# Optimization experiments

Measured on AMD Instinct MI355X. Metric: run time of the kernel, lower is better.

Reference implementation:

```python
import jax, jax.numpy as jnp
import numpy as np

N, E = 128, 2048
NODE_DIM, MSG_DIM, EDGE_DIM, ROUNDS, NUM_TYPES = 128, 128, 16, 2, 32


def setup_inputs() -> dict:
    key = jax.random.key(0)
    ks = jax.random.split(key, 10)
    s = 0.1  # weight scale to keep GRU numerics sane
    return {
        "node_types": jax.random.randint(ks[0], (N,), 0, NUM_TYPES),
        "src": jax.random.randint(ks[1], (E,), 0, N),
        "dst": jax.random.randint(ks[2], (E,), 0, N),
        "he": jax.random.normal(ks[3], (E, EDGE_DIM), jnp.float32),
        "enc_W": jax.random.normal(ks[4], (NODE_DIM, NUM_TYPES), jnp.float32) * s,
        "enc_b": jnp.zeros((NODE_DIM,), jnp.float32),
        "msg_W": jax.random.normal(ks[5], (ROUNDS, MSG_DIM, 2 * NODE_DIM + EDGE_DIM), jnp.float32) * s,
        "msg_b": jnp.zeros((ROUNDS, MSG_DIM), jnp.float32),
        "gru_Wih": jax.random.normal(ks[6], (ROUNDS, 3 * NODE_DIM, MSG_DIM), jnp.float32) * s,
        "gru_Whh": jax.random.normal(ks[7], (ROUNDS, 3 * NODE_DIM, NODE_DIM), jnp.float32) * s,
        "gru_bih": jnp.zeros((ROUNDS, 3 * NODE_DIM), jnp.float32),
        "gru_bhh": jnp.zeros((ROUNDS, 3 * NODE_DIM), jnp.float32),
        "cd_W": jax.random.normal(ks[8], (1, NODE_DIM), jnp.float32) * s,
        "cd_b": jnp.zeros((1,), jnp.float32),
    }


def _forward(node_types, src, dst, he, enc_W, enc_b, msg_W, msg_b,
             gru_Wih, gru_Whh, gru_bih, gru_bhh, cd_W, cd_b):
    n = node_types.shape[0]
    rounds = msg_W.shape[0]
    # initial_encoder on one-hot node types (g.ndata['out'].float())
    hv0 = jax.nn.one_hot(node_types, enc_W.shape[1], dtype=enc_W.dtype) @ enc_W.T + enc_b
    # fixed-key Gumbel noise emulating Categorical.sample() per destruction step
    gumbel = jax.random.gumbel(jax.random.key(42), (n - 1, n), dtype=hv0.dtype)

    def graph_prop(hv, alive):
        # DGL node removal emulated by alive mask; edges die with either endpoint
        emask = alive[src] & alive[dst]
        has_edges = emask.any()  # `if g.number_of_edges() > 0`
        emaskf = emask[:, None].astype(hv.dtype)
        upd = (has_edges & alive)[:, None]
        for t in range(rounds):
            m = jnp.concatenate([hv[src], hv[dst], he], axis=1)  # [E, 2d+e]
            m = (m @ msg_W[t].T + msg_b[t]) * emaskf             # [E, msg]
            a = jax.ops.segment_sum(m, dst, num_segments=n)      # [n, msg]; zero for no in-edges
            # torch.nn.GRUCell(a, hv), gate order r|z|n
            gi = a @ gru_Wih[t].T + gru_bih[t]
            gh = hv @ gru_Whh[t].T + gru_bhh[t]
            ir, iz, ih = jnp.split(gi, 3, axis=1)
            hr, hz, hn = jnp.split(gh, 3, axis=1)
            r = jax.nn.sigmoid(ir + hr)
            z = jax.nn.sigmoid(iz + hz)
            ncand = jnp.tanh(ih + r * hn)
            hv = jnp.where(upd, (1.0 - z) * ncand + z * hv, hv)
        return hv

    def step(carry, gn):
        hv, alive = carry
        hv = graph_prop(hv, alive)
        # softmax over dim=1 of [n,1] -> all ones (faithful to source); Categorical renormalizes
        probs = jax.nn.softmax(hv @ cd_W.T + cd_b, axis=1).reshape(-1)
        masked = probs * alive
        p = masked / masked.sum()
        vlog = jnp.where(alive, jnp.log(jnp.where(alive, p, 1.0)), -jnp.inf)
        victim = jnp.argmax(vlog + gn)  # Gumbel-max categorical sample
        logp = jnp.log(p[victim])
        alive = alive.at[victim].set(False)
        return (hv, alive), (victim, logp)

    alive0 = jnp.ones((n,), bool)
    (hv, alive), (victims, logps) = jax.lax.scan(step, (hv0, alive0), gumbel)
    survivor = jnp.argmax(alive)
    victim_order = jnp.concatenate([survivor[None], victims[::-1]])  # victim_order[::-1]
    return hv[survivor], victim_order, logps.sum()


def reference(node_types, src, dst, he, enc_W, enc_b, msg_W, msg_b,
              gru_Wih, gru_Whh, gru_bih, gru_bhh, cd_W, cd_b):
    return _forward(node_types, src, dst, he, enc_W, enc_b, msg_W, msg_b,
                    gru_Wih, gru_Whh, gru_bih, gru_bhh, cd_W, cd_b)
```

## Files before the change

kernel.cpp:

```cpp
#include <hip/hip_runtime.h>
#include <math.h>
#include <stdint.h>

#define STEPS 127
#define NBLK 64
#define NTHR 512
#define CAP 160

typedef unsigned int uint;

struct GDParams {
  const int* node_types; const int* esrc; const int* edst; const float* he;
  const float* enc_W; const float* enc_b; const float* msg_W; const float* msg_b;
  const float* Wih; const float* Whh; const float* bih; const float* bhh;
  unsigned* bar;
  unsigned* slots;
  float* buf0; float* buf1;
  float* g;
  unsigned short* Wp;
  float* W2T;
  float* bm2;
  float* HeSum;
  float* degs;
  unsigned char* alive;
  unsigned char* hasE;
  int* victims; int* row_ptr; int* in_count; int* cursor; int* col_src; int* col_eid;
  int* misc;
  float* out;
};

__device__ __forceinline__ void tfround(unsigned &x0, unsigned &x1, int r) {
  x0 += x1; x1 = (x1 << r) | (x1 >> (32 - r)); x1 ^= x0;
}
__device__ void threefry2x32(unsigned k0, unsigned k1, unsigned c0, unsigned c1,
                             unsigned &o0, unsigned &o1) {
  unsigned ks2 = k0 ^ k1 ^ 0x1BD11BDAu;
  unsigned x0 = c0 + k0, x1 = c1 + k1;
  tfround(x0,x1,13); tfround(x0,x1,15); tfround(x0,x1,26); tfround(x0,x1,6);
  x0 += k1; x1 += ks2 + 1u;
  tfround(x0,x1,17); tfround(x0,x1,29); tfround(x0,x1,16); tfround(x0,x1,24);
  x0 += ks2; x1 += k0 + 2u;
  tfround(x0,x1,13); tfround(x0,x1,15); tfround(x0,x1,26); tfround(x0,x1,6);
  x0 += k0; x1 += k1 + 3u;
  tfround(x0,x1,17); tfround(x0,x1,29); tfround(x0,x1,16); tfround(x0,x1,24);
  x0 += k1; x1 += ks2 + 4u;
  tfround(x0,x1,13); tfround(x0,x1,15); tfround(x0,x1,26); tfround(x0,x1,6);
  x0 += ks2; x1 += k0 + 5u;
  o0 = x0; o1 = x1;
}
__device__ __forceinline__ float gumbel_from_bits(unsigned b) {
  unsigned fb = (b >> 9) | 0x3F800000u;
  float f = __uint_as_float(fb) - 1.0f;
  const float tiny = 1.17549435e-38f;
  float u = fmaxf(tiny, f * (1.0f - tiny) + tiny);
  return -logf(-logf(u));
}

__device__ __forceinline__ unsigned short f2bf(float f) {
  unsigned u = __float_as_uint(f);
  unsigned r = (u + 0x7FFFu + ((u >> 16) & 1u)) >> 16;
  return (unsigned short)r;
}

#if __has_builtin(__builtin_amdgcn_fdot2_f32_bf16)
typedef __bf16 bf2 __attribute__((ext_vector_type(2)));
__device__ __forceinline__ float dot2bf(uint a, uint b, float c) {
  return __builtin_amdgcn_fdot2_f32_bf16(__builtin_bit_cast(bf2, a),
                                         __builtin_bit_cast(bf2, b), c, false);
}
#else
__device__ __forceinline__ float dot2bf(uint a, uint b, float c) {
  float a0 = __uint_as_float(a << 16), a1 = __uint_as_float(a & 0xFFFF0000u);
  float b0 = __uint_as_float(b << 16), b1 = __uint_as_float(b & 0xFFFF0000u);
  return fmaf(a0, b0, fmaf(a1, b1, c));
}
#endif

__device__ __forceinline__ float ld_dev(const float* a) {
  return __hip_atomic_load(const_cast<float*>(a), __ATOMIC_RELAXED, __HIP_MEMORY_SCOPE_AGENT);
}
__device__ __forceinline__ void st_dev(float* a, float v) {
  __hip_atomic_store(a, v, __ATOMIC_RELAXED, __HIP_MEMORY_SCOPE_AGENT);
}

__device__ __forceinline__ void gsync(unsigned* bar, unsigned &mygen) {
  __syncthreads();
  mygen++;
  if (threadIdx.x == 0) {
    unsigned prev = __hip_atomic_fetch_add(&bar[0], 1u, __ATOMIC_ACQ_REL, __HIP_MEMORY_SCOPE_AGENT);
    if (prev == (unsigned)(gridDim.x - 1u)) {
      __hip_atomic_store(&bar[0], 0u, __ATOMIC_RELAXED, __HIP_MEMORY_SCOPE_AGENT);
      __hip_atomic_store(&bar[1], mygen, __ATOMIC_RELEASE, __HIP_MEMORY_SCOPE_AGENT);
    } else {
      long guard = 0;
      while (__hip_atomic_load(&bar[1], __ATOMIC_ACQUIRE, __HIP_MEMORY_SCOPE_AGENT) != mygen) {
        if (++guard > (1L << 30)) break;
      }
    }
  }
  __syncthreads();
}

__device__ __forceinline__ void bpost(unsigned* slots, unsigned r) {
  __syncthreads();
  if (threadIdx.x == 0)
    __hip_atomic_store(&slots[blockIdx.x], r, __ATOMIC_RELAXED, __HIP_MEMORY_SCOPE_AGENT);
}
__device__ __forceinline__ void bwait(unsigned* slots, unsigned r) {
  if (threadIdx.x < 64) {
    long guard = 0;
    for (;;) {
      unsigned v = __hip_atomic_load(&slots[threadIdx.x], __ATOMIC_RELAXED, __HIP_MEMORY_SCOPE_AGENT);
      if (__all(v >= r)) break;
      if (++guard > (1L << 22)) break;
    }
  }
  __builtin_amdgcn_fence(__ATOMIC_ACQUIRE, "workgroup");
  __syncthreads();
}

__global__ __launch_bounds__(NTHR, 1) void gd_main(GDParams p) {
  __shared__ float pgq[4][2][384];
  __shared__ float pgr[2][2][384];
  __shared__ float pgh[2][2][384];
  __shared__ float pgHe[2][384];
  __shared__ alignas(16) unsigned short S_bf[2][128];
  __shared__ alignas(16) unsigned short hv_bf[2][128];
  __shared__ float hv_f[2][128];
  __shared__ int colL[2][CAP];
  __shared__ int cntL[2]; __shared__ int rpL[2];
  __shared__ float degL[2]; __shared__ int aliveL[2];
  __shared__ int victimL; __shared__ int hasEL;
  __shared__ int pfs[128];

  const int tid = threadIdx.x;
  const int gtid = blockIdx.x * NTHR + tid;
  const int GSZ = NBLK * NTHR;
  unsigned mygen = 0;

  if (blockIdx.x == 0) {
    for (int i = tid; i < 16256; i += NTHR) {
      unsigned o0, o1; threefry2x32(0u, 42u, 0u, (unsigned)i, o0, o1);
      p.g[i] = gumbel_from_bits(o0 ^ o1);
    }
    __syncthreads();
    if (tid < 64) {
      int lane = tid;
      bool a0 = true, a1 = true;
      float lsum = 0.f;
      for (int s = 0; s < STEPS; ++s) {
        p.alive[s * 128 + lane] = a0 ? 1 : 0;
        p.alive[s * 128 + 64 + lane] = a1 ? 1 : 0;
        float c = logf(1.0f / (float)(128 - s));
        float g0 = a0 ? (c + p.g[s * 128 + lane]) : -INFINITY;
        float g1 = a1 ? (c + p.g[s * 128 + 64 + lane]) : -INFINITY;
        float bv; int bi;
        if (g0 >= g1) { bv = g0; bi = lane; } else { bv = g1; bi = lane + 64; }
        for (int off = 32; off > 0; off >>= 1) {
          float ov = __shfl_down(bv, off);
          int   oi = __shfl_down(bi, off);
          if (ov > bv || (ov == bv && oi < bi)) { bv = ov; bi = oi; }
        }
        int victim = __shfl(bi, 0);
        if (victim == lane) a0 = false;
        if (victim == lane + 64) a1 = false;
        lsum += c;
        if (lane == 0) {
          p.victims[s] = victim;
          p.out[128 + 127 - s] = (float)victim;
        }
      }
      unsigned long long m0 = __ballot(a0), m1 = __ballot(a1);
      int surv = m0 ? (__ffsll(m0) - 1) : (64 + __ffsll(m1) - 1);
      if (lane == 0) { p.misc[0] = surv; p.out[128] = (float)surv; p.out[256] = lsum; }
    }
  } else {
    const int g63 = (blockIdx.x - 1) * NTHR + tid;
    const int GSZ63 = (NBLK - 1) * NTHR;
    for (int i = g63; i < 128; i += GSZ63) { p.in_count[i] = 0; p.cursor[i] = 0; }
    for (int i = g63; i < 16384; i += GSZ63) {
      int v = i >> 7, d = i & 127;
      p.buf0[i] = p.enc_W[d * 32 + p.node_types[v]] + p.enc_b[d];
    }
    for (int o = g63; o < 196608; o += GSZ63) {
      int mat = o / 98304; int r = o % 98304; int t = r / 49152; int rr = r % 49152;
      int k = rr / 384, j = rr % 384;
      const float* wih = p.Wih + (size_t)(t * 384 + j) * 128;
      const float* mw  = p.msg_W + (size_t)t * 128 * 272 + (mat * 128 + k);
      float acc = 0.f;
      for (int m = 0; m < 128; ++m) acc += wih[m] * mw[(size_t)m * 272];
      int mt = mat * 2 + t;
      p.Wp[(size_t)((mt * 16 + (k >> 3)) * 384 + j) * 8 + (k & 7)] = f2bf(acc);
    }
    for (int o = g63; o < 98304; o += GSZ63) {
      int t = o / 49152; int rr = o % 49152; int k = rr / 384, j = rr % 384;
      float acc = p.Whh[(size_t)(t * 384 + j) * 128 + k];
      int mt = 4 + t;
      p.Wp[(size_t)((mt * 16 + (k >> 3)) * 384 + j) * 8 + (k & 7)] = f2bf(acc);
    }
    for (int o = g63; o < 12288; o += GSZ63) {
      int t = o / 6144; int rr = o % 6144; int k = rr / 384, j = rr % 384;
      const float* wih = p.Wih + (size_t)(t * 384 + j) * 128;
      const float* mw  = p.msg_W + (size_t)t * 128 * 272 + (256 + k);
      float acc = 0.f;
      for (int m = 0; m < 128; ++m) acc += wih[m] * mw[(size_t)m * 272];
      p.W2T[(size_t)(t * 16 + k) * 384 + j] = acc;
    }
    for (int o = g63; o < 768; o += GSZ63) {
      int t = o / 384, j = o % 384;
      const float* wih = p.Wih + (size_t)(t * 384 + j) * 128;
      const float* mb = p.msg_b + t * 128;
      float acc = 0.f;
      for (int m = 0; m < 128; ++m) acc += wih[m] * mb[m];
      p.bm2[o] = acc;
    }
  }
  gsync(p.bar, mygen);

  if (blockIdx.x != 0) {
    for (int e = (blockIdx.x - 1) * NTHR + tid; e < 2048; e += (NBLK - 1) * NTHR)
      atomicAdd(&p.in_count[p.edst[e]], 1);
  }
  gsync(p.bar, mygen);

  if (blockIdx.x == 0) {
    if (tid < 128) pfs[tid] = p.in_count[tid];
    __syncthreads();
    for (int off = 1; off < 128; off <<= 1) {
      int add = 0;
      if (tid < 128 && tid >= off) add = pfs[tid - off];
      __syncthreads();
      if (tid < 128) pfs[tid] += add;
      __syncthreads();
    }
    if (tid == 0) p.row_ptr[0] = 0;
    if (tid < 128) p.row_ptr[tid + 1] = pfs[tid];
  }
  gsync(p.bar, mygen);

  for (int e = gtid; e < 2048; e += GSZ) {
    int dd = p.edst[e];
    int pos = atomicAdd(&p.cursor[dd], 1);
    int q = p.row_ptr[dd] + pos;
    p.col_src[q] = p.esrc[e];
    p.col_eid[q] = e;
  }
  gsync(p.bar, mygen);

  for (int i = gtid; i < 16256; i += GSZ) {
    int s = i >> 7, v = i & 127;
    int rp0 = p.row_ptr[v], rp1 = p.row_ptr[v + 1];
    const unsigned char* al = p.alive + s * 128;
    float deg = 0.f; float hacc[16];
    #pragma unroll
    for (int k = 0; k < 16; ++k) hacc[k] = 0.f;
    for (int q = rp0; q < rp1; ++q) {
      int u = p.col_src[q];
      if (al[u]) {
        deg += 1.f;
        const float* hr = p.he + (size_t)p.col_eid[q] * 16;
        #pragma unroll
        for (int k = 0; k < 16; ++k) hacc[k] += hr[k];
      }
    }
    p.degs[i] = deg;
    float* ho = p.HeSum + (size_t)i * 16;
    #pragma unroll
    for (int k = 0; k < 16; ++k) ho[k] = hacc[k];
  }
  gsync(p.bar, mygen);

  for (int s = gtid; s < STEPS; s += GSZ) {
    float acc = 0.f;
    for (int v = 0; v < 128; ++v)
      acc += p.alive[s * 128 + v] ? p.degs[s * 128 + v] : 0.f;
    p.hasE[s] = (acc > 0.f) ? 1 : 0;
  }
  for (int vv = 0; vv < 2; ++vv) {
    int v = blockIdx.x * 2 + vv;
    int rp0 = p.row_ptr[v], rp1 = p.row_ptr[v + 1];
    if (tid == 0) { cntL[vv] = rp1 - rp0; rpL[vv] = rp0; }
    int n = rp1 - rp0; if (n > CAP) n = CAP;
    for (int q = tid; q < n; q += NTHR) colL[vv][q] = p.col_src[rp0 + q];
  }
  gsync(p.bar, mygen);

  const float* cur = p.buf0; float* nxt = p.buf1;
  const int wave = tid >> 6, lane6 = tid & 63;
  const int nn = tid >> 7;
  const int dd_ = tid & 127;
  const int myv2 = blockIdx.x * 2;
  const uint4* Wp4 = (const uint4*)p.Wp;

  if (tid < 256) {
    float h0 = p.buf0[(size_t)(myv2 + nn) * 128 + dd_];
    hv_f[nn][dd_] = h0;
    hv_bf[nn][dd_] = f2bf(h0);
  }

  unsigned r = 0;
  for (int s = 0; s < STEPS; ++s) {
    for (int t = 0; t < 2; ++t) {
      r++;
      bpost(p.slots, r);

      if (wave >= 4) {
        const int m = 1 + ((wave - 4) >> 1);
        const int H = wave & 1;
        const uint4* WM = Wp4 + (size_t)(m * 2 + t) * 6144;
        float acc[6][2] = {};
        #pragma unroll
        for (int kc = 0; kc < 8; ++kc) {
          int kcg = H * 8 + kc;
          uint4 a0 = ((const uint4*)&hv_bf[0][0])[kcg];
          uint4 a1 = ((const uint4*)&hv_bf[1][0])[kcg];
          #pragma unroll
          for (int jj = 0; jj < 6; ++jj) {
            uint4 wv = WM[(size_t)kcg * 384 + lane6 + 64 * jj];
            acc[jj][0] = dot2bf(a0.x, wv.x, acc[jj][0]);
            acc[jj][0] = dot2bf(a0.y, wv.y, acc[jj][0]);
            acc[jj][0] = dot2bf(a0.z, wv.z, acc[jj][0]);
            acc[jj][0] = dot2bf(a0.w, wv.w, acc[jj][0]);
            acc[jj][1] = dot2bf(a1.x, wv.x, acc[jj][1]);
            acc[jj][1] = dot2bf(a1.y, wv.y, acc[jj][1]);
            acc[jj][1] = dot2bf(a1.z, wv.z, acc[jj][1]);
            acc[jj][1] = dot2bf(a1.w, wv.w, acc[jj][1]);
          }
        }
        float (*dst)[2][384] = (m == 1) ? pgr : pgh;
        #pragma unroll
        for (int jj = 0; jj < 6; ++jj) {
          dst[H][0][lane6 + 64 * jj] = acc[jj][0];
          dst[H][1][lane6 + 64 * jj] = acc[jj][1];
        }
        int base = tid - 256;
        #pragma unroll
        for (int ii = 0; ii < 3; ++ii) {
          int idx = base + 256 * ii;
          int n2 = (idx >= 384) ? 1 : 0;
          int j = idx - n2 * 384;
          int v = myv2 + n2;
          float deg = p.degs[s * 128 + v];
          float a = p.bih[t * 384 + j] + deg * p.bm2[t * 384 + j];
          const float* hs = p.HeSum + ((size_t)s * 128 + v) * 16;
          #pragma unroll
          for (int k2 = 0; k2 < 16; ++k2)
            a += hs[k2] * p.W2T[(size_t)(t * 16 + k2) * 384 + j];
          pgHe[n2][j] = a;
        }
      }

      bwait(p.slots, r);

      if (tid < 256) {
        if (tid == 0) { victimL = p.victims[s]; hasEL = p.hasE[s]; }
        if (dd_ == 0) {
          degL[nn] = p.degs[s * 128 + myv2 + nn];
          aliveL[nn] = p.alive[s * 128 + myv2 + nn];
        }
        float acc = 0.f;
        int cnt = cntL[nn];
        int cmin = cnt < CAP ? cnt : CAP;
        int q = 0;
        for (; q + 8 <= cmin; q += 8) {
          int u0 = colL[nn][q],   u1 = colL[nn][q+1], u2 = colL[nn][q+2], u3 = colL[nn][q+3];
          int u4 = colL[nn][q+4], u5 = colL[nn][q+5], u6 = colL[nn][q+6], u7 = colL[nn][q+7];
          float f0 = ld_dev(&cur[(size_t)u0*128 + dd_]);
          float f1 = ld_dev(&cur[(size_t)u1*128 + dd_]);
          float f2 = ld_dev(&cur[(size_t)u2*128 + dd_]);
          float f3 = ld_dev(&cur[(size_t)u3*128 + dd_]);
          float f4 = ld_dev(&cur[(size_t)u4*128 + dd_]);
          float f5 = ld_dev(&cur[(size_t)u5*128 + dd_]);
          float f6 = ld_dev(&cur[(size_t)u6*128 + dd_]);
          float f7 = ld_dev(&cur[(size_t)u7*128 + dd_]);
          acc += ((f0+f1)+(f2+f3)) + ((f4+f5)+(f6+f7));
        }
        for (; q < cnt; ++q) {
          int u = (q < CAP) ? colL[nn][q] : p.col_src[rpL[nn] + q];
          acc += ld_dev(&cur[(size_t)u*128 + dd_]);
        }
        S_bf[nn][dd_] = f2bf(acc);
      }
      __syncthreads();

      if (wave < 4) {
        const uint4* WQ = Wp4 + (size_t)(0 * 2 + t) * 6144;
        float acc[6][2] = {};
        #pragma unroll
        for (int kc = 0; kc < 4; ++kc) {
          int kcg = wave * 4 + kc;
          uint4 a0 = ((const uint4*)&S_bf[0][0])[kcg];
          uint4 a1 = ((const uint4*)&S_bf[1][0])[kcg];
          #pragma unroll
          for (int jj = 0; jj < 6; ++jj) {
            uint4 wv = WQ[(size_t)kcg * 384 + lane6 + 64 * jj];
            acc[jj][0] = dot2bf(a0.x, wv.x, acc[jj][0]);
            acc[jj][0] = dot2bf(a0.y, wv.y, acc[jj][0]);
            acc[jj][0] = dot2bf(a0.z, wv.z, acc[jj][0]);
            acc[jj][0] = dot2bf(a0.w, wv.w, acc[jj][0]);
            acc[jj][1] = dot2bf(a1.x, wv.x, acc[jj][1]);
            acc[jj][1] = dot2bf(a1.y, wv.y, acc[jj][1]);
            acc[jj][1] = dot2bf(a1.z, wv.z, acc[jj][1]);
            acc[jj][1] = dot2bf(a1.w, wv.w, acc[jj][1]);
          }
        }
        #pragma unroll
        for (int jj = 0; jj < 6; ++jj) {
          pgq[wave][0][lane6 + 64 * jj] = acc[jj][0];
          pgq[wave][1][lane6 + 64 * jj] = acc[jj][1];
        }
      }
      __syncthreads();

      if (tid < 256) {
        float deg = degL[nn];
        int j0 = dd_, j1 = 128 + dd_, j2 = 256 + dd_;
        float gir = pgq[0][nn][j0] + pgq[1][nn][j0] + pgq[2][nn][j0] + pgq[3][nn][j0]
                  + deg * (pgr[0][nn][j0] + pgr[1][nn][j0]) + pgHe[nn][j0];
        float giz = pgq[0][nn][j1] + pgq[1][nn][j1] + pgq[2][nn][j1] + pgq[3][nn][j1]
                  + deg * (pgr[0][nn][j1] + pgr[1][nn][j1]) + pgHe[nn][j1];
        float gin = pgq[0][nn][j2] + pgq[1][nn][j2] + pgq[2][nn][j2] + pgq[3][nn][j2]
                  + deg * (pgr[0][nn][j2] + pgr[1][nn][j2]) + pgHe[nn][j2];
        float ghr = pgh[0][nn][j0] + pgh[1][nn][j0] + p.bhh[t * 384 + j0];
        float ghz = pgh[0][nn][j1] + pgh[1][nn][j1] + p.bhh[t * 384 + j1];
        float ghn = pgh[0][nn][j2] + pgh[1][nn][j2] + p.bhh[t * 384 + j2];
        float rr_ = 1.f / (1.f + expf(-(gir + ghr)));
        float z = 1.f / (1.f + expf(-(giz + ghz)));
        float nc = tanhf(gin + rr_ * ghn);
        float old = hv_f[nn][dd_];
        bool upd = (hasEL != 0) && (aliveL[nn] != 0);
        float nv = upd ? (1.f - z) * nc + z * old : old;
        int myv = myv2 + nn;
        if (t == 1 && myv == victimL) nv = 0.f;
        st_dev(&nxt[(size_t)myv * 128 + dd_], nv);
        hv_f[nn][dd_] = nv;
        hv_bf[nn][dd_] = f2bf(nv);
      }
      const float* tmp = nxt; nxt = (float*)cur; cur = tmp;
    }
  }

  r++;
  bpost(p.slots, r);
  bwait(p.slots, r);
  if (blockIdx.x == 0 && tid < 128) {
    int surv = p.misc[0];
    p.out[tid] = ld_dev(&cur[(size_t)surv * 128 + tid]);
  }
}

extern "C" void kernel_launch(void* const* d_in, const int* in_sizes, int n_in,
                              void* d_out, int out_size, void* d_ws, size_t ws_size,
                              hipStream_t stream) {
  (void)in_sizes; (void)n_in; (void)out_size; (void)ws_size;
  GDParams p;
  p.node_types = (const int*)d_in[0];
  p.esrc = (const int*)d_in[1];
  p.edst = (const int*)d_in[2];
  p.he   = (const float*)d_in[3];
  p.enc_W = (const float*)d_in[4];
  p.enc_b = (const float*)d_in[5];
  p.msg_W = (const float*)d_in[6];
  p.msg_b = (const float*)d_in[7];
  p.Wih = (const float*)d_in[8];
  p.Whh = (const float*)d_in[9];
  p.bih = (const float*)d_in[10];
  p.bhh = (const float*)d_in[11];

  char* w = (char*)d_ws;
  auto take = [&](size_t n) { char* r = w; w += (n + 255) & ~(size_t)255; return r; };
  p.bar   = (unsigned*)take(256);
  p.slots = (unsigned*)take(256);
  p.buf0  = (float*)take(16384 * 4);
  p.buf1  = (float*)take(16384 * 4);
  p.g     = (float*)take(16256 * 4);
  p.Wp    = (unsigned short*)take((size_t)294912 * 2);
  p.W2T   = (float*)take(12288 * 4);
  p.bm2   = (float*)take(768 * 4);
  p.HeSum = (float*)take((size_t)16256 * 16 * 4);
  p.degs  = (float*)take(16256 * 4);
  p.alive = (unsigned char*)take(16384);
  p.hasE  = (unsigned char*)take(256);
  p.victims  = (int*)take(STEPS * 4);
  p.row_ptr  = (int*)take(129 * 4);
  p.in_count = (int*)take(128 * 4);
  p.cursor   = (int*)take(128 * 4);
  p.col_src  = (int*)take(2048 * 4);
  p.col_eid  = (int*)take(2048 * 4);
  p.misc     = (int*)take(256);
  p.out = (float*)d_out;

  (void)hipMemsetAsync(p.bar, 0, 512, stream);
  void* args[] = { (void*)&p };
  hipError_t err = hipLaunchCooperativeKernel(reinterpret_cast<void*>(gd_main),
                                              dim3(NBLK), dim3(NTHR), args, 0, stream);
  if (err != hipSuccess) {
    hipLaunchKernelGGL(gd_main, dim3(NBLK), dim3(NTHR), 0, stream, p);
  }
}
```

Before: 3.006 ms.

## Halve block count, pack hidden state as bf16, and early-exit finished blocks

New measurement: 4.410 ms. 46.7% more time.

```diff
diff --git a/kernel.cpp b/kernel.cpp
--- a/kernel.cpp
+++ b/kernel.cpp
@@ -3,7 +3,7 @@
 #include <stdint.h>
 
 #define STEPS 127
-#define NBLK 64
+#define NBLK 32
 #define NTHR 512
 #define CAP 160
 
@@ -15,7 +15,7 @@
   const float* Wih; const float* Whh; const float* bih; const float* bhh;
   unsigned* bar;
   unsigned* slots;
-  float* buf0; float* buf1;
+  uint* bufb0; uint* bufb1;
   float* g;
   unsigned short* Wp;
   float* W2T;
@@ -61,6 +61,8 @@
   unsigned r = (u + 0x7FFFu + ((u >> 16) & 1u)) >> 16;
   return (unsigned short)r;
 }
+__device__ __forceinline__ float bflo(uint w) { return __uint_as_float(w << 16); }
+__device__ __forceinline__ float bfhi(uint w) { return __uint_as_float(w & 0xFFFF0000u); }
 
 #if __has_builtin(__builtin_amdgcn_fdot2_f32_bf16)
 typedef __bf16 bf2 __attribute__((ext_vector_type(2)));
@@ -70,16 +72,14 @@
 }
 #else
 __device__ __forceinline__ float dot2bf(uint a, uint b, float c) {
-  float a0 = __uint_as_float(a << 16), a1 = __uint_as_float(a & 0xFFFF0000u);
-  float b0 = __uint_as_float(b << 16), b1 = __uint_as_float(b & 0xFFFF0000u);
-  return fmaf(a0, b0, fmaf(a1, b1, c));
+  return fmaf(bflo(a), bflo(b), fmaf(bfhi(a), bfhi(b), c));
 }
 #endif
 
-__device__ __forceinline__ float ld_dev(const float* a) {
-  return __hip_atomic_load(const_cast<float*>(a), __ATOMIC_RELAXED, __HIP_MEMORY_SCOPE_AGENT);
-}
-__device__ __forceinline__ void st_dev(float* a, float v) {
+__device__ __forceinline__ uint ld_devu(const uint* a) {
+  return __hip_atomic_load(const_cast<uint*>(a), __ATOMIC_RELAXED, __HIP_MEMORY_SCOPE_AGENT);
+}
+__device__ __forceinline__ void st_devu(uint* a, uint v) {
   __hip_atomic_store(a, v, __ATOMIC_RELAXED, __HIP_MEMORY_SCOPE_AGENT);
 }
 
@@ -108,11 +108,15 @@
 }
 __device__ __forceinline__ void bwait(unsigned* slots, unsigned r) {
   if (threadIdx.x < 64) {
+    int lane = threadIdx.x;
     long guard = 0;
     for (;;) {
-      unsigned v = __hip_atomic_load(&slots[threadIdx.x], __ATOMIC_RELAXED, __HIP_MEMORY_SCOPE_AGENT);
+      unsigned v = (lane < NBLK)
+        ? __hip_atomic_load(&slots[lane], __ATOMIC_RELAXED, __HIP_MEMORY_SCOPE_AGENT)
+        : 0xFFFFFFFFu;
       if (__all(v >= r)) break;
-      if (++guard > (1L << 22)) break;
+      __builtin_amdgcn_s_sleep(1);
+      if (++guard > (1L << 20)) break;
     }
   }
   __builtin_amdgcn_fence(__ATOMIC_ACQUIRE, "workgroup");
@@ -120,16 +124,16 @@
 }
 
 __global__ __launch_bounds__(NTHR, 1) void gd_main(GDParams p) {
-  __shared__ float pgq[4][2][384];
-  __shared__ float pgr[2][2][384];
-  __shared__ float pgh[2][2][384];
-  __shared__ float pgHe[2][384];
-  __shared__ alignas(16) unsigned short S_bf[2][128];
-  __shared__ alignas(16) unsigned short hv_bf[2][128];
-  __shared__ float hv_f[2][128];
-  __shared__ int colL[2][CAP];
-  __shared__ int cntL[2]; __shared__ int rpL[2];
-  __shared__ float degL[2]; __shared__ int aliveL[2];
+  __shared__ float pgq[4][4][384];
+  __shared__ float pgr[2][4][384];
+  __shared__ float pgh[2][4][384];
+  __shared__ float pgHe[4][384];
+  __shared__ alignas(16) uint S_u[4][64];
+  __shared__ alignas(16) uint hv_u[4][64];
+  __shared__ float hv_f[4][128];
+  __shared__ int colL[4][CAP];
+  __shared__ int cntL[4]; __shared__ int rpL[4];
+  __shared__ float degL[4]; __shared__ int aliveL[4];
   __shared__ int victimL; __shared__ int hasEL;
   __shared__ int pfs[128];
 
@@ -148,6 +152,7 @@
       int lane = tid;
       bool a0 = true, a1 = true;
       float lsum = 0.f;
+      p.misc[1 + lane] = 127; p.misc[1 + 64 + lane] = 127;
       for (int s = 0; s < STEPS; ++s) {
         p.alive[s * 128 + lane] = a0 ? 1 : 0;
         p.alive[s * 128 + 64 + lane] = a1 ? 1 : 0;
@@ -162,8 +167,8 @@
           if (ov > bv || (ov == bv && oi < bi)) { bv = ov; bi = oi; }
         }
         int victim = __shfl(bi, 0);
-        if (victim == lane) a0 = false;
-        if (victim == lane + 64) a1 = false;
+        if (victim == lane) { a0 = false; p.misc[1 + lane] = s; }
+        if (victim == lane + 64) { a1 = false; p.misc[1 + 64 + lane] = s; }
         lsum += c;
         if (lane == 0) {
           p.victims[s] = victim;
@@ -178,9 +183,12 @@
     const int g63 = (blockIdx.x - 1) * NTHR + tid;
     const int GSZ63 = (NBLK - 1) * NTHR;
     for (int i = g63; i < 128; i += GSZ63) { p.in_count[i] = 0; p.cursor[i] = 0; }
-    for (int i = g63; i < 16384; i += GSZ63) {
-      int v = i >> 7, d = i & 127;
-      p.buf0[i] = p.enc_W[d * 32 + p.node_types[v]] + p.enc_b[d];
+    for (int i = g63; i < 8192; i += GSZ63) {
+      int v = i >> 6, up = i & 63;
+      int ty = p.node_types[v];
+      float h0 = p.enc_W[(2 * up) * 32 + ty] + p.enc_b[2 * up];
+      float h1 = p.enc_W[(2 * up + 1) * 32 + ty] + p.enc_b[2 * up + 1];
+      p.bufb0[i] = (uint)f2bf(h0) | ((uint)f2bf(h1) << 16);
     }
     for (int o = g63; o < 196608; o += GSZ63) {
       int mat = o / 98304; int r = o % 98304; int t = r / 49152; int rr = r % 49152;
@@ -276,8 +284,8 @@
       acc += p.alive[s * 128 + v] ? p.degs[s * 128 + v] : 0.f;
     p.hasE[s] = (acc > 0.f) ? 1 : 0;
   }
-  for (int vv = 0; vv < 2; ++vv) {
-    int v = blockIdx.x * 2 + vv;
+  for (int vv = 0; vv < 4; ++vv) {
+    int v = blockIdx.x * 4 + vv;
     int rp0 = p.row_ptr[v], rp1 = p.row_ptr[v + 1];
     if (tid == 0) { cntL[vv] = rp1 - rp0; rpL[vv] = rp0; }
     int n = rp1 - rp0; if (n > CAP) n = CAP;
@@ -285,18 +293,28 @@
   }
   gsync(p.bar, mygen);
 
-  const float* cur = p.buf0; float* nxt = p.buf1;
+  const uint* curb = p.bufb0; uint* nxtb = p.bufb1;
   const int wave = tid >> 6, lane6 = tid & 63;
-  const int nn = tid >> 7;
-  const int dd_ = tid & 127;
-  const int myv2 = blockIdx.x * 2;
+  const int myv4 = blockIdx.x * 4;
   const uint4* Wp4 = (const uint4*)p.Wp;
 
-  if (tid < 256) {
-    float h0 = p.buf0[(size_t)(myv2 + nn) * 128 + dd_];
-    hv_f[nn][dd_] = h0;
-    hv_bf[nn][dd_] = f2bf(h0);
-  }
+  const int surv = p.misc[0];
+  int bexitS;
+  {
+    int m0 = p.misc[1 + myv4], m1 = p.misc[2 + myv4];
+    int m2 = p.misc[3 + myv4], m3 = p.misc[4 + myv4];
+    bexitS = max(max(m0, m1), max(m2, m3));
+  }
+
+  {
+    int n = tid >> 7, d = tid & 127;
+    int ty = p.node_types[myv4 + n];
+    float h0 = p.enc_W[d * 32 + ty] + p.enc_b[d];
+    hv_f[n][d] = h0;
+    float ph = __shfl_xor(h0, 1);
+    if ((tid & 1) == 0) hv_u[n][d >> 1] = (uint)f2bf(h0) | ((uint)f2bf(ph) << 16);
+  }
+  __syncthreads();
 
   unsigned r = 0;
   for (int s = 0; s < STEPS; ++s) {
@@ -304,16 +322,21 @@
       r++;
       bpost(p.slots, r);
 
-      if (wave >= 4) {
-        const int m = 1 + ((wave - 4) >> 1);
-        const int H = wave & 1;
-        const uint4* WM = Wp4 + (size_t)(m * 2 + t) * 6144;
+      if (tid == 0) { victimL = p.victims[s]; hasEL = p.hasE[s]; }
+      if (tid < 4) {
+        degL[tid] = p.degs[s * 128 + myv4 + tid];
+        aliveL[tid] = p.alive[s * 128 + myv4 + tid];
+      }
+      {
+        const int mm = wave & 1, H = (wave >> 1) & 1, P = wave >> 2;
+        const uint4* WM = Wp4 + (size_t)((mm ? 4 : 2) + t) * 6144;
+        const uint4* A0 = (const uint4*)&hv_u[P * 2][0];
+        const uint4* A1 = (const uint4*)&hv_u[P * 2 + 1][0];
         float acc[6][2] = {};
         #pragma unroll
         for (int kc = 0; kc < 8; ++kc) {
           int kcg = H * 8 + kc;
-          uint4 a0 = ((const uint4*)&hv_bf[0][0])[kcg];
-          uint4 a1 = ((const uint4*)&hv_bf[1][0])[kcg];
+          uint4 a0 = A0[kcg], a1 = A1[kcg];
           #pragma unroll
           for (int jj = 0; jj < 6; ++jj) {
             uint4 wv = WM[(size_t)kcg * 384 + lane6 + 64 * jj];
@@ -327,70 +350,72 @@
             acc[jj][1] = dot2bf(a1.w, wv.w, acc[jj][1]);
           }
         }
-        float (*dst)[2][384] = (m == 1) ? pgr : pgh;
+        float (*dst)[4][384] = mm ? pgh : pgr;
         #pragma unroll
         for (int jj = 0; jj < 6; ++jj) {
-          dst[H][0][lane6 + 64 * jj] = acc[jj][0];
-          dst[H][1][lane6 + 64 * jj] = acc[jj][1];
-        }
-        int base = tid - 256;
+          dst[H][P * 2][lane6 + 64 * jj] = acc[jj][0];
+          dst[H][P * 2 + 1][lane6 + 64 * jj] = acc[jj][1];
+        }
+      }
+      #pragma unroll
+      for (int ii = 0; ii < 3; ++ii) {
+        int idx = tid + 512 * ii;
+        int n2 = idx / 384, j = idx - n2 * 384;
+        int v = myv4 + n2;
+        float dg = p.degs[s * 128 + v];
+        float a = p.bih[t * 384 + j] + dg * p.bm2[t * 384 + j];
+        const float* hs = p.HeSum + ((size_t)s * 128 + v) * 16;
         #pragma unroll
-        for (int ii = 0; ii < 3; ++ii) {
-          int idx = base + 256 * ii;
-          int n2 = (idx >= 384) ? 1 : 0;
-          int j = idx - n2 * 384;
-          int v = myv2 + n2;
-          float deg = p.degs[s * 128 + v];
-          float a = p.bih[t * 384 + j] + deg * p.bm2[t * 384 + j];
-          const float* hs = p.HeSum + ((size_t)s * 128 + v) * 16;
-          #pragma unroll
-          for (int k2 = 0; k2 < 16; ++k2)
-            a += hs[k2] * p.W2T[(size_t)(t * 16 + k2) * 384 + j];
-          pgHe[n2][j] = a;
-        }
+        for (int k2 = 0; k2 < 16; ++k2)
+          a += hs[k2] * p.W2T[(size_t)(t * 16 + k2) * 384 + j];
+        pgHe[n2][j] = a;
       }
 
       bwait(p.slots, r);
 
-      if (tid < 256) {
-        if (tid == 0) { victimL = p.victims[s]; hasEL = p.hasE[s]; }
-        if (dd_ == 0) {
-          degL[nn] = p.degs[s * 128 + myv2 + nn];
-          aliveL[nn] = p.alive[s * 128 + myv2 + nn];
-        }
-        float acc = 0.f;
-        int cnt = cntL[nn];
+      {
+        int n = tid >> 7, u = (tid >> 1) & 63, e = tid & 1;
+        int cnt = cntL[n];
         int cmin = cnt < CAP ? cnt : CAP;
-        int q = 0;
-        for (; q + 8 <= cmin; q += 8) {
-          int u0 = colL[nn][q],   u1 = colL[nn][q+1], u2 = colL[nn][q+2], u3 = colL[nn][q+3];
-          int u4 = colL[nn][q+4], u5 = colL[nn][q+5], u6 = colL[nn][q+6], u7 = colL[nn][q+7];
-          float f0 = ld_dev(&cur[(size_t)u0*128 + dd_]);
-          float f1 = ld_dev(&cur[(size_t)u1*128 + dd_]);
-          float f2 = ld_dev(&cur[(size_t)u2*128 + dd_]);
-          float f3 = ld_dev(&cur[(size_t)u3*128 + dd_]);
-          float f4 = ld_dev(&cur[(size_t)u4*128 + dd_]);
-          float f5 = ld_dev(&cur[(size_t)u5*128 + dd_]);
-          float f6 = ld_dev(&cur[(size_t)u6*128 + dd_]);
-          float f7 = ld_dev(&cur[(size_t)u7*128 + dd_]);
-          acc += ((f0+f1)+(f2+f3)) + ((f4+f5)+(f6+f7));
-        }
-        for (; q < cnt; ++q) {
-          int u = (q < CAP) ? colL[nn][q] : p.col_src[rpL[nn] + q];
-          acc += ld_dev(&cur[(size_t)u*128 + dd_]);
-        }
-        S_bf[nn][dd_] = f2bf(acc);
+        float aL = 0.f, aH = 0.f;
+        int q = e;
+        for (; q + 14 < cmin; q += 16) {
+          int c0 = colL[n][q],      c1 = colL[n][q + 2],  c2 = colL[n][q + 4],  c3 = colL[n][q + 6];
+          int c4 = colL[n][q + 8],  c5 = colL[n][q + 10], c6 = colL[n][q + 12], c7 = colL[n][q + 14];
+          uint w0 = ld_devu(&curb[(size_t)c0 * 64 + u]);
+          uint w1 = ld_devu(&curb[(size_t)c1 * 64 + u]);
+          uint w2 = ld_devu(&curb[(size_t)c2 * 64 + u]);
+          uint w3 = ld_devu(&curb[(size_t)c3 * 64 + u]);
+          uint w4 = ld_devu(&curb[(size_t)c4 * 64 + u]);
+          uint w5 = ld_devu(&curb[(size_t)c5 * 64 + u]);
+          uint w6 = ld_devu(&curb[(size_t)c6 * 64 + u]);
+          uint w7 = ld_devu(&curb[(size_t)c7 * 64 + u]);
+          aL += ((bflo(w0) + bflo(w1)) + (bflo(w2) + bflo(w3)))
+              + ((bflo(w4) + bflo(w5)) + (bflo(w6) + bflo(w7)));
+          aH += ((bfhi(w0) + bfhi(w1)) + (bfhi(w2) + bfhi(w3)))
+              + ((bfhi(w4) + bfhi(w5)) + (bfhi(w6) + bfhi(w7)));
+        }
+        for (; q < cnt; q += 2) {
+          int c = (q < CAP) ? colL[n][q] : p.col_src[rpL[n] + q];
+          uint w = ld_devu(&curb[(size_t)c * 64 + u]);
+          aL += bflo(w); aH += bfhi(w);
+        }
+        aL += __shfl_xor(aL, 1);
+        aH += __shfl_xor(aH, 1);
+        if (e == 0) S_u[n][u] = (uint)f2bf(aL) | ((uint)f2bf(aH) << 16);
       }
       __syncthreads();
 
-      if (wave < 4) {
-        const uint4* WQ = Wp4 + (size_t)(0 * 2 + t) * 6144;
+      {
+        const int qq = wave & 3, P = (wave >> 2) & 1;
+        const uint4* WQ = Wp4 + (size_t)t * 6144;
+        const uint4* A0 = (const uint4*)&S_u[P * 2][0];
+        const uint4* A1 = (const uint4*)&S_u[P * 2 + 1][0];
         float acc[6][2] = {};
         #pragma unroll
         for (int kc = 0; kc < 4; ++kc) {
-          int kcg = wave * 4 + kc;
-          uint4 a0 = ((const uint4*)&S_bf[0][0])[kcg];
-          uint4 a1 = ((const uint4*)&S_bf[1][0])[kcg];
+          int kcg = qq * 4 + kc;
+          uint4 a0 = A0[kcg], a1 = A1[kcg];
           #pragma unroll
           for (int jj = 0; jj < 6; ++jj) {
             uint4 wv = WQ[(size_t)kcg * 384 + lane6 + 64 * jj];
@@ -406,46 +431,55 @@
         }
         #pragma unroll
         for (int jj = 0; jj < 6; ++jj) {
-          pgq[wave][0][lane6 + 64 * jj] = acc[jj][0];
-          pgq[wave][1][lane6 + 64 * jj] = acc[jj][1];
+          pgq[qq][P * 2][lane6 + 64 * jj] = acc[jj][0];
+          pgq[qq][P * 2 + 1][lane6 + 64 * jj] = acc[jj][1];
         }
       }
       __syncthreads();
 
-      if (tid < 256) {
-        float deg = degL[nn];
-        int j0 = dd_, j1 = 128 + dd_, j2 = 256 + dd_;
-        float gir = pgq[0][nn][j0] + pgq[1][nn][j0] + pgq[2][nn][j0] + pgq[3][nn][j0]
-                  + deg * (pgr[0][nn][j0] + pgr[1][nn][j0]) + pgHe[nn][j0];
-        float giz = pgq[0][nn][j1] + pgq[1][nn][j1] + pgq[2][nn][j1] + pgq[3][nn][j1]
-                  + deg * (pgr[0][nn][j1] + pgr[1][nn][j1]) + pgHe[nn][j1];
-        float gin = pgq[0][nn][j2] + pgq[1][nn][j2] + pgq[2][nn][j2] + pgq[3][nn][j2]
-                  + deg * (pgr[0][nn][j2] + pgr[1][nn][j2]) + pgHe[nn][j2];
-        float ghr = pgh[0][nn][j0] + pgh[1][nn][j0] + p.bhh[t * 384 + j0];
-        float ghz = pgh[0][nn][j1] + pgh[1][nn][j1] + p.bhh[t * 384 + j1];
-        float ghn = pgh[0][nn][j2] + pgh[1][nn][j2] + p.bhh[t * 384 + j2];
+      {
+        int n = tid >> 7, d = tid & 127;
+        float deg = degL[n];
+        int j0 = d, j1 = 128 + d, j2 = 256 + d;
+        float gir = pgq[0][n][j0] + pgq[1][n][j0] + pgq[2][n][j0] + pgq[3][n][j0]
+                  + deg * (pgr[0][n][j0] + pgr[1][n][j0]) + pgHe[n][j0];
+        float giz = pgq[0][n][j1] + pgq[1][n][j1] + pgq[2][n][j1] + pgq[3][n][j1]
+                  + deg * (pgr[0][n][j1] + pgr[1][n][j1]) + pgHe[n][j1];
+        float gin = pgq[0][n][j2] + pgq[1][n][j2] + pgq[2][n][j2] + pgq[3][n][j2]
+                  + deg * (pgr[0][n][j2] + pgr[1][n][j2]) + pgHe[n][j2];
+        float ghr = pgh[0][n][j0] + pgh[1][n][j0] + p.bhh[t * 384 + j0];
+        float ghz = pgh[0][n][j1] + pgh[1][n][j1] + p.bhh[t * 384 + j1];
+        float ghn = pgh[0][n][j2] + pgh[1][n][j2] + p.bhh[t * 384 + j2];
         float rr_ = 1.f / (1.f + expf(-(gir + ghr)));
         float z = 1.f / (1.f + expf(-(giz + ghz)));
         float nc = tanhf(gin + rr_ * ghn);
-        float old = hv_f[nn][dd_];
-        bool upd = (hasEL != 0) && (aliveL[nn] != 0);
+        float old = hv_f[n][d];
+        bool upd = (hasEL != 0) && (aliveL[n] != 0);
         float nv = upd ? (1.f - z) * nc + z * old : old;
-        int myv = myv2 + nn;
-        if (t == 1 && myv == victimL) nv = 0.f;
-        st_dev(&nxt[(size_t)myv * 128 + dd_], nv);
-        hv_f[nn][dd_] = nv;
-        hv_bf[nn][dd_] = f2bf(nv);
-      }
-      const float* tmp = nxt; nxt = (float*)cur; cur = tmp;
-    }
-  }
-
-  r++;
-  bpost(p.slots, r);
-  bwait(p.slots, r);
-  if (blockIdx.x == 0 && tid < 128) {
-    int surv = p.misc[0];
-    p.out[tid] = ld_dev(&cur[(size_t)surv * 128 + tid]);
+        if (t == 1 && (myv4 + n) == victimL) nv = 0.f;
+        hv_f[n][d] = nv;
+        float pnv = __shfl_xor(nv, 1);
+        if ((tid & 1) == 0) {
+          uint pk = (uint)f2bf(nv) | ((uint)f2bf(pnv) << 16);
+          hv_u[n][d >> 1] = pk;
+          st_devu(&nxtb[(size_t)(myv4 + n) * 64 + (d >> 1)], pk);
+        }
+      }
+
+      if (t == 1 && s == bexitS) {
+        if (tid < 256) st_devu((uint*)&curb[(size_t)(myv4 + (tid >> 6)) * 64 + (tid & 63)], 0u);
+        __syncthreads();
+        if (tid == 0)
+          __hip_atomic_store(&p.slots[blockIdx.x], 0x7FFFFFFFu, __ATOMIC_RELAXED, __HIP_MEMORY_SCOPE_AGENT);
+        return;
+      }
+
+      const uint* tmp = nxtb; nxtb = (uint*)curb; curb = tmp;
+    }
+  }
+
+  if ((surv >> 2) == (int)blockIdx.x && tid < 128) {
+    p.out[tid] = hv_f[surv & 3][tid];
   }
 }
 
@@ -471,8 +505,8 @@
   auto take = [&](size_t n) { char* r = w; w += (n + 255) & ~(size_t)255; return r; };
   p.bar   = (unsigned*)take(256);
   p.slots = (unsigned*)take(256);
-  p.buf0  = (float*)take(16384 * 4);
-  p.buf1  = (float*)take(16384 * 4);
+  p.bufb0 = (uint*)take(8192 * 4);
+  p.bufb1 = (uint*)take(8192 * 4);
   p.g     = (float*)take(16256 * 4);
   p.Wp    = (unsigned short*)take((size_t)294912 * 2);
   p.W2T   = (float*)take(12288 * 4);
@@ -487,7 +521,7 @@
   p.cursor   = (int*)take(128 * 4);
   p.col_src  = (int*)take(2048 * 4);
   p.col_eid  = (int*)take(2048 * 4);
-  p.misc     = (int*)take(256);
+  p.misc     = (int*)take(1024);
   p.out = (float*)d_out;
 
   (void)hipMemsetAsync(p.bar, 0, 512, stream);
```
